# Kernel tuning notes

Measured on AMD Instinct MI355X. Metric: run time of the kernel, lower is better.

Reference implementation:

```python
import jax, jax.numpy as jnp
import numpy as np

VOXEL_RES = 4
CLASSES = 40


def setup_inputs() -> dict:
    key = jax.random.key(0)
    kx, kw, kb = jax.random.split(key, 3)
    B, N = 64, 100000
    x = jax.random.normal(kx, (B, N, 3), dtype=jnp.float32)
    F = VOXEL_RES ** 3
    bound = 1.0 / np.sqrt(F)  # torch Linear default init range
    W = jax.random.uniform(kw, (CLASSES, F), minval=-bound, maxval=bound, dtype=jnp.float32)
    b = jax.random.uniform(kb, (CLASSES,), minval=-bound, maxval=bound, dtype=jnp.float32)
    return {"x": x, "W": W, "b": b}


def reference(x, W, b):
    # x: (B, N, 3). Faithful to torch.histogramdd(bins=R): the histogram range
    # per dimension is [min, max] of the data; the last bin is right-inclusive.
    B, N, _ = x.shape
    R = VOXEL_RES
    mn = jnp.min(x, axis=1, keepdims=True)  # (B, 1, 3)
    mx = jnp.max(x, axis=1, keepdims=True)  # (B, 1, 3)
    # bin index = floor((v - min) / (max - min) * R), clipped so v == max -> R-1
    idx = jnp.floor((x - mn) / (mx - mn) * R).astype(jnp.int32)
    idx = jnp.clip(idx, 0, R - 1)  # (B, N, 3)
    flat = idx[..., 0] * R * R + idx[..., 1] * R + idx[..., 2]  # (B, N)
    flat = flat + (jnp.arange(B, dtype=jnp.int32) * (R ** 3))[:, None]
    counts = jax.ops.segment_sum(
        jnp.ones((B * N,), dtype=x.dtype), flat.reshape(-1), num_segments=B * R ** 3
    ).reshape(B, R ** 3)
    counts = counts / N  # fraction of points per voxel
    class_outputs = counts @ W.T + b  # (B, classes)
    return class_outputs
```

## Files before the change

### kernel.cpp

```cpp
#include <hip/hip_runtime.h>

#define VR 4
#define NVOX 64
#define NCLS 40
#define NB 64
#define NPTS 100000
#define BPB 16
#define NBLK (NB * BPB)
#define G_PER_B (NPTS / 4)
#define F4_PER_B (NPTS * 3 / 4)
#define STRIDE_G (BPB * 256)
#define FULL_ITERS (G_PER_B / STRIDE_G)
#define NT_ITERS 4
#define TAIL_G (G_PER_B - FULL_ITERS * STRIDE_G)
#define SW_LD 41
#define FLT_BIG 3.402823466e38f

typedef float f4 __attribute__((ext_vector_type(4)));

static __device__ __forceinline__ int bin1(float v, float mn, float s4) {
    int i = (int)((v - mn) * s4);
    return i > (VR - 1) ? (VR - 1) : i;
}

static __device__ __forceinline__ unsigned long long vox_mask(
        int v, const unsigned long long* ns) {
    return (__ballot(v & 1)  ^ ns[0]) & (__ballot(v & 2)  ^ ns[1])
         & (__ballot(v & 4)  ^ ns[2]) & (__ballot(v & 8)  ^ ns[3])
         & (__ballot(v & 16) ^ ns[4]) & (__ballot(v & 32) ^ ns[5]);
}


__global__ __launch_bounds__(256) void minmax_k(const f4* __restrict__ x,
                                                float* __restrict__ pmin,
                                                float* __restrict__ pmax,
                                                float* __restrict__ out) {
    const int bid = blockIdx.x;
    const int b = bid & (NB - 1);
    const int sub = bid >> 6;
    const f4* xb = x + (size_t)b * F4_PER_B;
    const int lane = threadIdx.x & 63;
    const int wv = threadIdx.x >> 6;
    const int t0 = sub * 256 + (int)threadIdx.x;

    if (sub == 0 && threadIdx.x < NCLS)
        out[b * NCLS + threadIdx.x] = 0.f;

    float mn0 = FLT_BIG, mn1 = FLT_BIG, mn2 = FLT_BIG;
    float mx0 = -FLT_BIG, mx1 = -FLT_BIG, mx2 = -FLT_BIG;
    #pragma unroll
    for (int k = 0; k < FULL_ITERS; k++) {
        const int g = t0 + k * STRIDE_G;
        f4 a, c, e;
        if (k < NT_ITERS) {
            a = __builtin_nontemporal_load(&xb[3 * g]);
            c = __builtin_nontemporal_load(&xb[3 * g + 1]);
            e = __builtin_nontemporal_load(&xb[3 * g + 2]);
        } else {
            a = xb[3 * g]; c = xb[3 * g + 1]; e = xb[3 * g + 2];
        }
        mn0 = fminf(mn0, fminf(fminf(a[0], a[3]), fminf(c[2], e[1])));
        mx0 = fmaxf(mx0, fmaxf(fmaxf(a[0], a[3]), fmaxf(c[2], e[1])));
        mn1 = fminf(mn1, fminf(fminf(a[1], c[0]), fminf(c[3], e[2])));
        mx1 = fmaxf(mx1, fmaxf(fmaxf(a[1], c[0]), fmaxf(c[3], e[2])));
        mn2 = fminf(mn2, fminf(fminf(a[2], c[1]), fminf(e[0], e[3])));
        mx2 = fmaxf(mx2, fmaxf(fmaxf(a[2], c[1]), fmaxf(e[0], e[3])));
    }
    if (sub * 256 < TAIL_G && t0 < TAIL_G) {
        const int g = FULL_ITERS * STRIDE_G + t0;
        const f4 a = xb[3 * g], c = xb[3 * g + 1], e = xb[3 * g + 2];
        mn0 = fminf(mn0, fminf(fminf(a[0], a[3]), fminf(c[2], e[1])));
        mx0 = fmaxf(mx0, fmaxf(fmaxf(a[0], a[3]), fmaxf(c[2], e[1])));
        mn1 = fminf(mn1, fminf(fminf(a[1], c[0]), fminf(c[3], e[2])));
        mx1 = fmaxf(mx1, fmaxf(fmaxf(a[1], c[0]), fmaxf(c[3], e[2])));
        mn2 = fminf(mn2, fminf(fminf(a[2], c[1]), fminf(e[0], e[3])));
        mx2 = fmaxf(mx2, fmaxf(fmaxf(a[2], c[1]), fmaxf(e[0], e[3])));
    }

    #pragma unroll
    for (int off = 32; off > 0; off >>= 1) {
        mn0 = fminf(mn0, __shfl_down(mn0, off, 64));
        mn1 = fminf(mn1, __shfl_down(mn1, off, 64));
        mn2 = fminf(mn2, __shfl_down(mn2, off, 64));
        mx0 = fmaxf(mx0, __shfl_down(mx0, off, 64));
        mx1 = fmaxf(mx1, __shfl_down(mx1, off, 64));
        mx2 = fmaxf(mx2, __shfl_down(mx2, off, 64));
    }

    __shared__ float smn[4][3], smx[4][3];
    if (lane == 0) {
        smn[wv][0] = mn0; smn[wv][1] = mn1; smn[wv][2] = mn2;
        smx[wv][0] = mx0; smx[wv][1] = mx1; smx[wv][2] = mx2;
    }
    __syncthreads();
    if (threadIdx.x < 3) {
        const int d = threadIdx.x;
        float a = smn[0][d], z = smx[0][d];
        #pragma unroll
        for (int w = 1; w < 4; w++) {
            a = fminf(a, smn[w][d]);
            z = fmaxf(z, smx[w][d]);
        }
        pmin[(b * BPB + sub) * 3 + d] = a;
        pmax[(b * BPB + sub) * 3 + d] = z;
    }
}

__global__ __launch_bounds__(256, 4) void hist_gemv_k(const f4* __restrict__ x,
                                                      const float* __restrict__ pmin,
                                                      const float* __restrict__ pmax,
                                                      const float* __restrict__ W,
                                                      const float* __restrict__ bias,
                                                      float* __restrict__ out) {
    const int bid = blockIdx.x;
    const int b = bid & (NB - 1);
    const int sub = bid >> 6;
    const f4* xb = x + (size_t)b * F4_PER_B;
    const int lane = threadIdx.x & 63;
    const int wv = threadIdx.x >> 6;
    const int t0 = sub * 256 + (int)threadIdx.x;

    __shared__ float sW[NVOX * SW_LD];
    __shared__ float smm[6];
    __shared__ unsigned swh[4][NVOX];
    __shared__ float fh[NVOX];

    f4 A[FULL_ITERS], C[FULL_ITERS], E[FULL_ITERS];
    #pragma unroll
    for (int k = FULL_ITERS - 1; k >= 0; k--) {
        const int g = t0 + k * STRIDE_G;
        A[k] = xb[3 * g]; C[k] = xb[3 * g + 1]; E[k] = xb[3 * g + 2];
    }

    for (int i = threadIdx.x; i < NCLS * NVOX; i += 256)
        sW[(i % NVOX) * SW_LD + (i / NVOX)] = W[i];
    if (threadIdx.x < 6) {
        const int d = threadIdx.x % 3;
        const bool isMax = threadIdx.x >= 3;
        float r = isMax ? -FLT_BIG : FLT_BIG;
        for (int s = 0; s < BPB; s++) {
            float v = isMax ? pmax[(b * BPB + s) * 3 + d]
                            : pmin[(b * BPB + s) * 3 + d];
            r = isMax ? fmaxf(r, v) : fminf(r, v);
        }
        smm[threadIdx.x] = r;
    }
    __syncthreads();
    const float bn0 = smm[0], bn1 = smm[1], bn2 = smm[2];
    const float s40 = (float)VR / (smm[3] - smm[0]);
    const float s41 = (float)VR / (smm[4] - smm[1]);
    const float s42 = (float)VR / (smm[5] - smm[2]);

    unsigned long long ns[6];
    #pragma unroll
    for (int k = 0; k < 6; k++)
        ns[k] = ((lane >> k) & 1) ? 0ull : ~0ull;

    unsigned cnt = 0;
    if (sub * 256 < TAIL_G) {
        const bool valid = t0 < TAIL_G;
        const unsigned long long vm = __ballot(valid);
        const int g = FULL_ITERS * STRIDE_G + (valid ? t0 : 0);
        const f4 a = xb[3 * g], c = xb[3 * g + 1], e = xb[3 * g + 2];
        int v0 = bin1(a[0], bn0, s40) * 16 + bin1(a[1], bn1, s41) * 4 + bin1(a[2], bn2, s42);
        int v1 = bin1(a[3], bn0, s40) * 16 + bin1(c[0], bn1, s41) * 4 + bin1(c[1], bn2, s42);
        int v2 = bin1(c[2], bn0, s40) * 16 + bin1(c[3], bn1, s41) * 4 + bin1(e[0], bn2, s42);
        int v3 = bin1(e[1], bn0, s40) * 16 + bin1(e[2], bn1, s41) * 4 + bin1(e[3], bn2, s42);
        cnt += (unsigned)__popcll(vm & vox_mask(v0, ns));
        cnt += (unsigned)__popcll(vm & vox_mask(v1, ns));
        cnt += (unsigned)__popcll(vm & vox_mask(v2, ns));
        cnt += (unsigned)__popcll(vm & vox_mask(v3, ns));
    }
    #pragma unroll
    for (int k = FULL_ITERS - 1; k >= 0; k--) {
        const f4 a = A[k], c = C[k], e = E[k];
        int v0 = bin1(a[0], bn0, s40) * 16 + bin1(a[1], bn1, s41) * 4 + bin1(a[2], bn2, s42);
        int v1 = bin1(a[3], bn0, s40) * 16 + bin1(c[0], bn1, s41) * 4 + bin1(c[1], bn2, s42);
        int v2 = bin1(c[2], bn0, s40) * 16 + bin1(c[3], bn1, s41) * 4 + bin1(e[0], bn2, s42);
        int v3 = bin1(e[1], bn0, s40) * 16 + bin1(e[2], bn1, s41) * 4 + bin1(e[3], bn2, s42);
        cnt += (unsigned)__popcll(vox_mask(v0, ns));
        cnt += (unsigned)__popcll(vox_mask(v1, ns));
        cnt += (unsigned)__popcll(vox_mask(v2, ns));
        cnt += (unsigned)__popcll(vox_mask(v3, ns));
    }

    swh[wv][lane] = cnt;
    __syncthreads();
    if (threadIdx.x < NVOX)
        fh[threadIdx.x] = (float)(swh[0][threadIdx.x] + swh[1][threadIdx.x] +
                                  swh[2][threadIdx.x] + swh[3][threadIdx.x])
                          * (1.0f / (float)NPTS);
    __syncthreads();
    if (threadIdx.x < NCLS) {
        const int c = threadIdx.x;
        float acc = (sub == 0) ? bias[c] : 0.f;
        #pragma unroll
        for (int f = 0; f < NVOX; f++)
            acc += fh[f] * sW[f * SW_LD + c];
        atomicAdd(&out[b * NCLS + c], acc);
    }
}

extern "C" void kernel_launch(void* const* d_in, const int* in_sizes, int n_in,
                              void* d_out, int out_size, void* d_ws, size_t ws_size,
                              hipStream_t stream) {
    const f4* x = (const f4*)d_in[0];
    const float* W = (const float*)d_in[1];
    const float* bias = (const float*)d_in[2];
    float* out = (float*)d_out;

    float* pmin = (float*)d_ws;
    float* pmax = pmin + NBLK * 3;

    minmax_k<<<NBLK, 256, 0, stream>>>(x, pmin, pmax, out);
    hist_gemv_k<<<NBLK, 256, 0, stream>>>(x, pmin, pmax, W, bias, out);
}
```

Baseline: 128.1 us.

## Load points inside histogram loop instead of prefetching all into registers

The histogram kernel no longer preloads every full-iteration point group into register arrays before waiting on the min/max reduction. It now loads each group inside a partially unrolled loop, keeping only the tail load ahead of the barrier. The min/max kernel drops its nontemporal loads for the early iterations, and the histogram kernel's minimum-occupancy launch bound is removed. This lowers register pressure but gives up overlapping the global loads with the W staging and min/max reduce, and may lose L2 reuse of x between the two kernels if the cache hints mattered.

```diff
diff --git a/kernel.cpp b/kernel.cpp
--- a/kernel.cpp
+++ b/kernel.cpp
@@ -11,7 +11,6 @@
 #define F4_PER_B (NPTS * 3 / 4)
 #define STRIDE_G (BPB * 256)
 #define FULL_ITERS (G_PER_B / STRIDE_G)
-#define NT_ITERS 4
 #define TAIL_G (G_PER_B - FULL_ITERS * STRIDE_G)
 #define SW_LD 41
 #define FLT_BIG 3.402823466e38f
@@ -51,14 +50,7 @@
     #pragma unroll
     for (int k = 0; k < FULL_ITERS; k++) {
         const int g = t0 + k * STRIDE_G;
-        f4 a, c, e;
-        if (k < NT_ITERS) {
-            a = __builtin_nontemporal_load(&xb[3 * g]);
-            c = __builtin_nontemporal_load(&xb[3 * g + 1]);
-            e = __builtin_nontemporal_load(&xb[3 * g + 2]);
-        } else {
-            a = xb[3 * g]; c = xb[3 * g + 1]; e = xb[3 * g + 2];
-        }
+        const f4 a = xb[3 * g], c = xb[3 * g + 1], e = xb[3 * g + 2];
         mn0 = fminf(mn0, fminf(fminf(a[0], a[3]), fminf(c[2], e[1])));
         mx0 = fmaxf(mx0, fmaxf(fmaxf(a[0], a[3]), fmaxf(c[2], e[1])));
         mn1 = fminf(mn1, fminf(fminf(a[1], c[0]), fminf(c[3], e[2])));
@@ -106,12 +98,12 @@
     }
 }
 
-__global__ __launch_bounds__(256, 4) void hist_gemv_k(const f4* __restrict__ x,
-                                                      const float* __restrict__ pmin,
-                                                      const float* __restrict__ pmax,
-                                                      const float* __restrict__ W,
-                                                      const float* __restrict__ bias,
-                                                      float* __restrict__ out) {
+__global__ __launch_bounds__(256) void hist_gemv_k(const f4* __restrict__ x,
+                                                   const float* __restrict__ pmin,
+                                                   const float* __restrict__ pmax,
+                                                   const float* __restrict__ W,
+                                                   const float* __restrict__ bias,
+                                                   float* __restrict__ out) {
     const int bid = blockIdx.x;
     const int b = bid & (NB - 1);
     const int sub = bid >> 6;
@@ -125,11 +117,12 @@
     __shared__ unsigned swh[4][NVOX];
     __shared__ float fh[NVOX];
 
-    f4 A[FULL_ITERS], C[FULL_ITERS], E[FULL_ITERS];
-    #pragma unroll
-    for (int k = FULL_ITERS - 1; k >= 0; k--) {
-        const int g = t0 + k * STRIDE_G;
-        A[k] = xb[3 * g]; C[k] = xb[3 * g + 1]; E[k] = xb[3 * g + 2];
+    const bool hasTail = (sub * 256 < TAIL_G);
+    const bool tailValid = hasTail && (t0 < TAIL_G);
+    f4 ta = {0,0,0,0}, tc = {0,0,0,0}, te = {0,0,0,0};
+    if (hasTail) {
+        const int g = FULL_ITERS * STRIDE_G + (tailValid ? t0 : 0);
+        ta = xb[3 * g]; tc = xb[3 * g + 1]; te = xb[3 * g + 2];
     }
 
     for (int i = threadIdx.x; i < NCLS * NVOX; i += 256)
@@ -157,23 +150,21 @@
         ns[k] = ((lane >> k) & 1) ? 0ull : ~0ull;
 
     unsigned cnt = 0;
-    if (sub * 256 < TAIL_G) {
-        const bool valid = t0 < TAIL_G;
-        const unsigned long long vm = __ballot(valid);
-        const int g = FULL_ITERS * STRIDE_G + (valid ? t0 : 0);
-        const f4 a = xb[3 * g], c = xb[3 * g + 1], e = xb[3 * g + 2];
-        int v0 = bin1(a[0], bn0, s40) * 16 + bin1(a[1], bn1, s41) * 4 + bin1(a[2], bn2, s42);
-        int v1 = bin1(a[3], bn0, s40) * 16 + bin1(c[0], bn1, s41) * 4 + bin1(c[1], bn2, s42);
-        int v2 = bin1(c[2], bn0, s40) * 16 + bin1(c[3], bn1, s41) * 4 + bin1(e[0], bn2, s42);
-        int v3 = bin1(e[1], bn0, s40) * 16 + bin1(e[2], bn1, s41) * 4 + bin1(e[3], bn2, s42);
+    if (hasTail) {
+        const unsigned long long vm = __ballot(tailValid);
+        int v0 = bin1(ta[0], bn0, s40) * 16 + bin1(ta[1], bn1, s41) * 4 + bin1(ta[2], bn2, s42);
+        int v1 = bin1(ta[3], bn0, s40) * 16 + bin1(tc[0], bn1, s41) * 4 + bin1(tc[1], bn2, s42);
+        int v2 = bin1(tc[2], bn0, s40) * 16 + bin1(tc[3], bn1, s41) * 4 + bin1(te[0], bn2, s42);
+        int v3 = bin1(te[1], bn0, s40) * 16 + bin1(te[2], bn1, s41) * 4 + bin1(te[3], bn2, s42);
         cnt += (unsigned)__popcll(vm & vox_mask(v0, ns));
         cnt += (unsigned)__popcll(vm & vox_mask(v1, ns));
         cnt += (unsigned)__popcll(vm & vox_mask(v2, ns));
         cnt += (unsigned)__popcll(vm & vox_mask(v3, ns));
     }
-    #pragma unroll
+    #pragma unroll 2
     for (int k = FULL_ITERS - 1; k >= 0; k--) {
-        const f4 a = A[k], c = C[k], e = E[k];
+        const int g = t0 + k * STRIDE_G;
+        const f4 a = xb[3 * g], c = xb[3 * g + 1], e = xb[3 * g + 2];
         int v0 = bin1(a[0], bn0, s40) * 16 + bin1(a[1], bn1, s41) * 4 + bin1(a[2], bn2, s42);
         int v1 = bin1(a[3], bn0, s40) * 16 + bin1(c[0], bn1, s41) * 4 + bin1(c[1], bn2, s42);
         int v2 = bin1(c[2], bn0, s40) * 16 + bin1(c[3], bn1, s41) * 4 + bin1(e[0], bn2, s42);
```

New measurement: 123.6 us. -3.5%, faster.
